# Kernel optimization log

Measured on AMD Instinct MI355X. Metric: run time of the kernel, lower is better.

Reference implementation:

```python
import jax, jax.numpy as jnp
import numpy as np

B, S, H = 2, 1024, 2048
E, K, F = 64, 8, 768
CAP = 512


def setup_inputs() -> dict:
    key = jax.random.key(0)
    k1, k2, k3, k4, k5 = jax.random.split(key, 5)
    scale_h = 1.0 / np.sqrt(H)
    scale_f = 1.0 / np.sqrt(F)
    return {
        "hidden_states": jax.random.normal(k1, (B, S, H), jnp.float32),
        "router_w": jax.random.normal(k2, (E, H), jnp.float32) * scale_h,   # MoEGate.weight [E, H]
        "w_gate": jax.random.normal(k3, (E, H, F), jnp.float32) * scale_h,
        "w_up": jax.random.normal(k4, (E, H, F), jnp.float32) * scale_h,
        "w_down": jax.random.normal(k5, (E, F, H), jnp.float32) * scale_f,
    }


def reference(hidden_states, router_w, w_gate, w_up, w_down):
    b, s, h = hidden_states.shape
    T = b * s
    xf = hidden_states.reshape(T, h)

    # --- MoEGate: softmax over expert logits, then top-k, then renormalize ---
    logits = xf @ router_w.T                                   # [T, E]
    scores = jax.nn.softmax(logits.astype(jnp.float32), axis=-1)
    topk_w, topk_idx = jax.lax.top_k(scores, K)                # [T, K]
    topk_w = topk_w / (topk_w.sum(axis=-1, keepdims=True) + 1e-20)

    # --- dispatch: scatter each (token, k) slot into a per-expert capacity buffer ---
    slot_expert = topk_idx.reshape(-1)                         # [T*K]
    slot_token = jnp.repeat(jnp.arange(T), K)                  # [T*K]
    onehot = jax.nn.one_hot(slot_expert, E, dtype=jnp.int32)   # [T*K, E]
    pos = (jnp.cumsum(onehot, axis=0) * onehot).sum(-1) - 1    # position within expert
    valid = pos < CAP
    dest = jnp.where(valid, slot_expert * CAP + pos, E * CAP)  # overflow -> dummy row

    buf = jnp.zeros((E * CAP + 1, h), xf.dtype).at[dest].set(xf[slot_token])
    xb = buf[: E * CAP].reshape(E, CAP, h)                     # [E, CAP, H]

    # --- grouped GEMM experts: SwiGLU MLP per expert ---
    gate = jnp.einsum("ech,ehf->ecf", xb, w_gate)
    up = jnp.einsum("ech,ehf->ecf", xb, w_up)
    hmid = jax.nn.silu(gate) * up                              # [E, CAP, F]
    yb = jnp.einsum("ecf,efh->ech", hmid, w_down).reshape(E * CAP, h)
    yb = jnp.concatenate([yb, jnp.zeros((1, h), yb.dtype)], axis=0)

    # --- combine: gather expert outputs back, weight, scatter-add per token ---
    slot_out = yb[dest] * topk_w.reshape(-1)[:, None].astype(yb.dtype)
    out = jnp.zeros((T, h), yb.dtype).at[slot_token].add(slot_out)
    return out.reshape(b, s, h)
```

## Files before the change

kernel.cpp:

```cpp
#include <hip/hip_runtime.h>
#include <math.h>

#define T_TOK 2048
#define HD    2048
#define NEXP  64
#define KTOP  8
#define FD    768
#define CAPE  512

typedef float  f32x4 __attribute__((ext_vector_type(4)));
typedef __bf16 bf16x8 __attribute__((ext_vector_type(8)));
typedef __bf16 bf16x4 __attribute__((ext_vector_type(4)));

__device__ __forceinline__ void load_lds16(const void* g, void* l) {
  __builtin_amdgcn_global_load_lds(
      (const __attribute__((address_space(1))) unsigned int*)g,
      (__attribute__((address_space(3))) unsigned int*)l, 16, 0, 0);
}

#define WAITCNT(S) asm volatile(S ::: "memory")
#define PIN()      asm volatile("" ::: "memory")
#define BARRIER()  __builtin_amdgcn_s_barrier()

__global__ __launch_bounds__(256) void router_kernel(
    const float* __restrict__ x, const float* __restrict__ rw,
    int* __restrict__ cnt, int* __restrict__ tok_list, float* __restrict__ w_list,
    unsigned short* __restrict__ xb)
{
  const int t = threadIdx.x;
  const int tb = blockIdx.x * 4;
  __shared__ float xs[4][HD];
  __shared__ float lg[4][NEXP];

  const float4* xsrc = (const float4*)(x + (size_t)tb * HD);
  float4* xdst = (float4*)&xs[0][0];
  for (int i = t; i < 4 * HD / 4; i += 256) xdst[i] = xsrc[i];
  __syncthreads();

  {
    const int e = t >> 2, q = t & 3;
    const float* wrow = rw + (size_t)e * HD;
    float a0 = 0.f, a1 = 0.f, a2 = 0.f, a3 = 0.f;
    for (int i = 0; i < HD / 16; ++i) {
      int h = (i * 4 + q) * 4;
      float4 wv = *(const float4*)(wrow + h);
      float4 x0 = *(const float4*)&xs[0][h];
      float4 x1 = *(const float4*)&xs[1][h];
      float4 x2 = *(const float4*)&xs[2][h];
      float4 x3 = *(const float4*)&xs[3][h];
      a0 += wv.x*x0.x + wv.y*x0.y + wv.z*x0.z + wv.w*x0.w;
      a1 += wv.x*x1.x + wv.y*x1.y + wv.z*x1.z + wv.w*x1.w;
      a2 += wv.x*x2.x + wv.y*x2.y + wv.z*x2.z + wv.w*x2.w;
      a3 += wv.x*x3.x + wv.y*x3.y + wv.z*x3.z + wv.w*x3.w;
    }
    a0 += __shfl_xor(a0, 1); a0 += __shfl_xor(a0, 2);
    a1 += __shfl_xor(a1, 1); a1 += __shfl_xor(a1, 2);
    a2 += __shfl_xor(a2, 1); a2 += __shfl_xor(a2, 2);
    a3 += __shfl_xor(a3, 1); a3 += __shfl_xor(a3, 2);
    if (q == 0) { lg[0][e] = a0; lg[1][e] = a1; lg[2][e] = a2; lg[3][e] = a3; }
  }

  {
    const f32x4* xs4 = (const f32x4*)(x + (size_t)tb * HD);
    bf16x4* xbd = (bf16x4*)(xb + (size_t)tb * HD);
    #pragma unroll
    for (int j = 0; j < 8; ++j) {
      f32x4 v = xs4[j * 256 + t];
      xbd[j * 256 + t] = (bf16x4){(__bf16)v[0], (__bf16)v[1], (__bf16)v[2], (__bf16)v[3]};
    }
  }
  __syncthreads();

  const int wid = t >> 6, lane = t & 63;
  float v = lg[wid][lane];
  float mx = v;
  for (int o = 32; o; o >>= 1) mx = fmaxf(mx, __shfl_xor(mx, o));
  float p = expf(v - mx);
  float s = p;
  for (int o = 32; o; o >>= 1) s += __shfl_xor(s, o);
  float prob = p / s;

  float r = prob;
  float wk[KTOP]; int ik[KTOP]; float wsum = 0.f;
  #pragma unroll
  for (int k = 0; k < KTOP; ++k) {
    float bv = r; int bl = lane;
    for (int o = 32; o; o >>= 1) {
      float ov = __shfl_xor(bv, o); int ol = __shfl_xor(bl, o);
      if (ov > bv || (ov == bv && ol < bl)) { bv = ov; bl = ol; }
    }
    wk[k] = bv; ik[k] = bl; wsum += bv;
    if (lane == bl) r = -1.f;
  }
  if (lane == 0) {
    float inv = 1.f / (wsum + 1e-20f);
    int token = tb + wid;
    #pragma unroll
    for (int k = 0; k < KTOP; ++k) {
      int ex = ik[k];
      int pos = atomicAdd(&cnt[ex], 1);
      if (pos < CAPE) {
        tok_list[ex * CAPE + pos] = token;
        w_list[ex * CAPE + pos] = wk[k] * inv;
      }
    }
  }
}


__global__ __launch_bounds__(512, 4) void gateup_kernel(
    const unsigned short* __restrict__ xb,
    const float* __restrict__ wg, const float* __restrict__ wu,
    const int* __restrict__ cnt, const int* __restrict__ tok_list,
    unsigned short* __restrict__ hmid)
{
  const int nt = blockIdx.x, mt = blockIdx.y, e = blockIdx.z;
  int ne = cnt[e]; ne = ne < CAPE ? ne : CAPE;
  if (mt * 128 >= ne) return;
  const int t = threadIdx.x, lane = t & 63, wid = t >> 6;
  const int wr = wid >> 1, wc = wid & 1;

  __shared__ __align__(16) unsigned short A[2 * 128 * 64];
  __shared__ __align__(16) unsigned short Bg[64 * 72];
  __shared__ __align__(16) unsigned short Bu[64 * 72];
  __shared__ int toks[128];

  if (t < 128) {
    int r = mt * 128 + t;
    toks[t] = tok_list[e * CAPE + (r < ne ? r : 0)];
  }
  __syncthreads();

  const unsigned short* asrc[2];
  #pragma unroll
  for (int i = 0; i < 2; ++i) {
    const int inst = wid * 2 + i;
    const int G = inst * 64 + lane;
    const int m = G >> 3, gg = G & 7;
    asrc[i] = xb + (size_t)toks[m] * HD + 8 * (gg ^ (m & 7));
  }

  f32x4 z4 = {0.f, 0.f, 0.f, 0.f};
  f32x4 gacc[2][2], uacc[2][2];
  #pragma unroll
  for (int i = 0; i < 2; ++i)
    #pragma unroll
    for (int j = 0; j < 2; ++j) { gacc[i][j] = z4; uacc[i][j] = z4; }

  const int bq = t & 255, nc = bq & 15, kc = bq >> 4;
  const float* wsel = (wid < 4) ? wg : wu;
  __bf16* bsel = (wid < 4) ? (__bf16*)Bg : (__bf16*)Bu;
  const size_t wbase = (size_t)e * HD * FD + (size_t)nt * 64;
  f32x4 Ra[4], Rb[4];

#define LOAD_GU(K0, R) do { \
    const float* p_ = wsel + wbase + (size_t)((K0) + kc * 4) * FD + nc * 4; \
    R[0] = *(const f32x4*)p_;            R[1] = *(const f32x4*)(p_ + FD); \
    R[2] = *(const f32x4*)(p_ + 2*FD);   R[3] = *(const f32x4*)(p_ + 3*FD); \
  } while (0)

#define STAGE_A2(KT, BUF) do { \
    const int k0s_ = (KT) * 64; \
    load_lds16(asrc[0] + k0s_, &A[(BUF) * 8192 + (wid * 2 + 0) * 512]); \
    load_lds16(asrc[1] + k0s_, &A[(BUF) * 8192 + (wid * 2 + 1) * 512]); \
  } while (0)

#define CVT_GU(R) do { \
    const int xm_ = (nc & 7) << 3; \
    _Pragma("unroll") \
    for (int j_ = 0; j_ < 4; ++j_) { \
      int so_ = (nc * 4 + j_) * 72 + ((kc * 4) ^ xm_); \
      *(bf16x4*)&bsel[so_] = (bf16x4){(__bf16)R[0][j_], (__bf16)R[1][j_], (__bf16)R[2][j_], (__bf16)R[3][j_]}; \
    } \
  } while (0)

#define COMPUTE_GU(CUR) do { \
    const char* Ab_ = (const char*)&A[(CUR) * 8192]; \
    const __bf16* Bg_ = (const __bf16*)Bg; \
    const __bf16* Bu_ = (const __bf16*)Bu; \
    _Pragma("unroll") \
    for (int ks = 0; ks < 2; ++ks) { \
      bf16x8 af[2]; \
      _Pragma("unroll") \
      for (int mf = 0; mf < 2; ++mf) { \
        int row = wr * 32 + mf * 16 + (lane & 15); \
        int byte = row * 128 + (lane >> 4) * 16 + ks * 64; \
        byte ^= (row & 7) << 4; \
        af[mf] = *(const bf16x8*)(Ab_ + byte); \
      } \
      _Pragma("unroll") \
      for (int nf = 0; nf < 2; ++nf) { \
        int n = wc * 32 + nf * 16 + (lane & 15); \
        int so = n * 72 + ((((lane >> 4) * 8) + ks * 32) ^ (((n >> 2) & 7) << 3)); \
        bf16x8 bgf = *(const bf16x8*)&Bg_[so]; \
        bf16x8 bum = *(const bf16x8*)&Bu_[so]; \
        _Pragma("unroll") \
        for (int mf = 0; mf < 2; ++mf) { \
          gacc[mf][nf] = __builtin_amdgcn_mfma_f32_16x16x32_bf16(af[mf], bgf, gacc[mf][nf], 0, 0, 0); \
          uacc[mf][nf] = __builtin_amdgcn_mfma_f32_16x16x32_bf16(af[mf], bum, uacc[mf][nf], 0, 0, 0); \
        } \
      } \
    } \
  } while (0)

  LOAD_GU(0, Ra);
  PIN();
  STAGE_A2(0, 0);
  PIN();
  LOAD_GU(64, Rb);
  WAITCNT("s_waitcnt vmcnt(6)");
  CVT_GU(Ra);
  WAITCNT("s_waitcnt vmcnt(4) lgkmcnt(0)");
  BARRIER();

  for (int i = 0; i < 15; ++i) {
    const int kt = 2 * i;
    STAGE_A2(kt + 1, 1);
    PIN();
    LOAD_GU((kt + 2) * 64, Ra);
    COMPUTE_GU(0);
    WAITCNT("s_waitcnt lgkmcnt(0)");
    BARRIER();
    WAITCNT("s_waitcnt vmcnt(6)");
    CVT_GU(Rb);
    WAITCNT("s_waitcnt vmcnt(4) lgkmcnt(0)");
    BARRIER();
    STAGE_A2(kt + 2, 0);
    PIN();
    LOAD_GU((kt + 3) * 64, Rb);
    COMPUTE_GU(1);
    WAITCNT("s_waitcnt lgkmcnt(0)");
    BARRIER();
    WAITCNT("s_waitcnt vmcnt(6)");
    CVT_GU(Ra);
    WAITCNT("s_waitcnt vmcnt(4) lgkmcnt(0)");
    BARRIER();
  }
  STAGE_A2(31, 1);
  COMPUTE_GU(0);
  WAITCNT("s_waitcnt lgkmcnt(0)");
  BARRIER();
  WAITCNT("s_waitcnt vmcnt(2)");
  CVT_GU(Rb);
  WAITCNT("s_waitcnt vmcnt(0) lgkmcnt(0)");
  BARRIER();
  COMPUTE_GU(1);

#undef LOAD_GU
#undef STAGE_A2
#undef CVT_GU
#undef COMPUTE_GU

  const size_t hbase = (size_t)e * CAPE + (size_t)mt * 128;
  __bf16* hm = (__bf16*)hmid;
  #pragma unroll
  for (int mf = 0; mf < 2; ++mf) {
    #pragma unroll
    for (int nf = 0; nf < 2; ++nf) {
      #pragma unroll
      for (int r = 0; r < 4; ++r) {
        int row = wr * 32 + mf * 16 + (lane >> 4) * 4 + r;
        int c = nt * 64 + wc * 32 + nf * 16 + (lane & 15);
        float gv = gacc[mf][nf][r], uv = uacc[mf][nf][r];
        float hv = gv / (1.f + __expf(-gv)) * uv;
        hm[(hbase + row) * FD + c] = (__bf16)hv;
      }
    }
  }
}

__global__ __launch_bounds__(512, 4) void down_kernel(
    const unsigned short* __restrict__ hmid,
    const float* __restrict__ wd,
    const int* __restrict__ cnt, const int* __restrict__ tok_list,
    const float* __restrict__ w_list, float* __restrict__ out)
{
  const int nt = blockIdx.x, mt = blockIdx.y, e = blockIdx.z;
  int ne = cnt[e]; ne = ne < CAPE ? ne : CAPE;
  if (mt * 128 >= ne) return;
  const int t = threadIdx.x, lane = t & 63, wid = t >> 6;
  const int wr = wid >> 1, wc = wid & 1;

  __shared__ __align__(16) unsigned short A[2 * 128 * 64];
  __shared__ __align__(16) unsigned short Bd[64 * 72];
  __shared__ int toks[128];
  __shared__ float wts[128];

  if (t < 128) {
    int r = mt * 128 + t;
    bool vv = r < ne;
    toks[t] = vv ? tok_list[e * CAPE + r] : 0;
    wts[t]  = vv ? w_list[e * CAPE + r] : 0.f;
  }
  __syncthreads();

  const size_t arow = (size_t)e * CAPE + (size_t)mt * 128;
  const unsigned short* asrc[2];
  #pragma unroll
  for (int i = 0; i < 2; ++i) {
    const int inst = wid * 2 + i;
    const int G = inst * 64 + lane;
    const int m = G >> 3, gg = G & 7;
    asrc[i] = hmid + (arow + m) * FD + 8 * (gg ^ (m & 7));
  }

  f32x4 z4 = {0.f, 0.f, 0.f, 0.f};
  f32x4 dacc[2][2];
  #pragma unroll
  for (int i = 0; i < 2; ++i)
    #pragma unroll
    for (int j = 0; j < 2; ++j) dacc[i][j] = z4;

  const int bq = t & 255, nc = bq & 15, kc = bq >> 4;
  const size_t wbase = (size_t)e * FD * HD + (size_t)nt * 64;
  f32x4 Ra[4], Rb[4];

#define LOAD_D(K0, R) do { \
    const float* p_ = wd + wbase + (size_t)((K0) + kc * 4) * HD + nc * 4; \
    R[0] = *(const f32x4*)p_;            R[1] = *(const f32x4*)(p_ + HD); \
    R[2] = *(const f32x4*)(p_ + 2*HD);   R[3] = *(const f32x4*)(p_ + 3*HD); \
  } while (0)

#define STAGE_A2(KT, BUF) do { \
    const int k0s_ = (KT) * 64; \
    load_lds16(asrc[0] + k0s_, &A[(BUF) * 8192 + (wid * 2 + 0) * 512]); \
    load_lds16(asrc[1] + k0s_, &A[(BUF) * 8192 + (wid * 2 + 1) * 512]); \
  } while (0)

#define CVT_D(R) do { \
    __bf16* bd_ = (__bf16*)Bd; \
    const int xm_ = (nc & 7) << 3; \
    _Pragma("unroll") \
    for (int j_ = 0; j_ < 4; ++j_) { \
      int so_ = (nc * 4 + j_) * 72 + ((kc * 4) ^ xm_); \
      *(bf16x4*)&bd_[so_] = (bf16x4){(__bf16)R[0][j_], (__bf16)R[1][j_], (__bf16)R[2][j_], (__bf16)R[3][j_]}; \
    } \
  } while (0)

#define COMPUTE_D(CUR) do { \
    const char* Ab_ = (const char*)&A[(CUR) * 8192]; \
    const __bf16* Bd_ = (const __bf16*)Bd; \
    _Pragma("unroll") \
    for (int ks = 0; ks < 2; ++ks) { \
      bf16x8 af[2]; \
      _Pragma("unroll") \
      for (int mf = 0; mf < 2; ++mf) { \
        int row = wr * 32 + mf * 16 + (lane & 15); \
        int byte = row * 128 + (lane >> 4) * 16 + ks * 64; \
        byte ^= (row & 7) << 4; \
        af[mf] = *(const bf16x8*)(Ab_ + byte); \
      } \
      _Pragma("unroll") \
      for (int nf = 0; nf < 2; ++nf) { \
        int n = wc * 32 + nf * 16 + (lane & 15); \
        int so = n * 72 + ((((lane >> 4) * 8) + ks * 32) ^ (((n >> 2) & 7) << 3)); \
        bf16x8 bdf = *(const bf16x8*)&Bd_[so]; \
        _Pragma("unroll") \
        for (int mf = 0; mf < 2; ++mf) \
          dacc[mf][nf] = __builtin_amdgcn_mfma_f32_16x16x32_bf16(af[mf], bdf, dacc[mf][nf], 0, 0, 0); \
      } \
    } \
  } while (0)

  if (wid < 4) LOAD_D(0, Ra);
  PIN();
  STAGE_A2(0, 0);
  PIN();
  if (wid < 4) {
    LOAD_D(64, Rb);
    WAITCNT("s_waitcnt vmcnt(6)");
    CVT_D(Ra);
    WAITCNT("s_waitcnt vmcnt(4) lgkmcnt(0)");
  } else {
    WAITCNT("s_waitcnt vmcnt(0) lgkmcnt(0)");
  }
  BARRIER();

  for (int i = 0; i < 5; ++i) {
    const int kt = 2 * i;
    STAGE_A2(kt + 1, 1);
    PIN();
    if (wid < 4) LOAD_D((kt + 2) * 64, Ra);
    COMPUTE_D(0);
    WAITCNT("s_waitcnt lgkmcnt(0)");
    BARRIER();
    if (wid < 4) {
      WAITCNT("s_waitcnt vmcnt(6)");
      CVT_D(Rb);
      WAITCNT("s_waitcnt vmcnt(4) lgkmcnt(0)");
    } else {
      WAITCNT("s_waitcnt vmcnt(0) lgkmcnt(0)");
    }
    BARRIER();

    STAGE_A2(kt + 2, 0);
    PIN();
    if (wid < 4) LOAD_D((kt + 3) * 64, Rb);
    COMPUTE_D(1);
    WAITCNT("s_waitcnt lgkmcnt(0)");
    BARRIER();
    if (wid < 4) {
      WAITCNT("s_waitcnt vmcnt(6)");
      CVT_D(Ra);
      WAITCNT("s_waitcnt vmcnt(4) lgkmcnt(0)");
    } else {
      WAITCNT("s_waitcnt vmcnt(0) lgkmcnt(0)");
    }
    BARRIER();
  }
  STAGE_A2(11, 1);
  COMPUTE_D(0);
  WAITCNT("s_waitcnt lgkmcnt(0)");
  BARRIER();
  if (wid < 4) {
    WAITCNT("s_waitcnt vmcnt(2)");
    CVT_D(Rb);
    WAITCNT("s_waitcnt vmcnt(0) lgkmcnt(0)");
  } else {
    WAITCNT("s_waitcnt vmcnt(0) lgkmcnt(0)");
  }
  BARRIER();
  COMPUTE_D(1);

#undef LOAD_D
#undef STAGE_A2
#undef CVT_D
#undef COMPUTE_D

  #pragma unroll
  for (int mf = 0; mf < 2; ++mf) {
    #pragma unroll
    for (int nf = 0; nf < 2; ++nf) {
      int c = nt * 64 + wc * 32 + nf * 16 + (lane & 15);
      #pragma unroll
      for (int r = 0; r < 4; ++r) {
        int row = wr * 32 + mf * 16 + (lane >> 4) * 4 + r;
        if (mt * 128 + row < ne) {
          int tok = toks[row];
          float w = wts[row];
          atomicAdd(&out[(size_t)tok * HD + c], w * dacc[mf][nf][r]);
        }
      }
    }
  }
}

extern "C" void kernel_launch(void* const* d_in, const int* in_sizes, int n_in,
                              void* d_out, int out_size, void* d_ws, size_t ws_size,
                              hipStream_t stream) {
  const float* x  = (const float*)d_in[0];
  const float* rw = (const float*)d_in[1];
  const float* wg = (const float*)d_in[2];
  const float* wu = (const float*)d_in[3];
  const float* wd = (const float*)d_in[4];
  float* out = (float*)d_out;

  char* ws = (char*)d_ws;
  unsigned short* xb   = (unsigned short*)ws;
  int* cnt             = (int*)(ws + 8388608);
  int* tok_list        = (int*)(ws + 8388864);
  float* w_list        = (float*)(ws + 8519936);
  unsigned short* hmid = (unsigned short*)(ws + 8651008);

  hipMemsetAsync(d_out, 0, (size_t)out_size * sizeof(float), stream);
  hipMemsetAsync(cnt, 0, NEXP * sizeof(int), stream);

  router_kernel<<<T_TOK / 4, 256, 0, stream>>>(x, rw, cnt, tok_list, w_list, xb);
  gateup_kernel<<<dim3(FD / 64, CAPE / 128, NEXP), 512, 0, stream>>>(xb, wg, wu, cnt, tok_list, hmid);
  down_kernel<<<dim3(HD / 64, CAPE / 128, NEXP), 512, 0, stream>>>(hmid, wd, cnt, tok_list, w_list, out);
}
```

Baseline: 706.9 us.

## Double-buffer weight LDS tiles, remap block order for XCD locality, spread down loads

Gives the B (weight) tiles in both MoE GEMM kernels two LDS buffers, so the bf16 conversion of the next tile overlaps the MFMA compute on the current one. This removes one barrier per k-step. Block IDs are flattened into a 1D grid and remapped so consecutive blocks on the same XCD (bid&7) cover neighbouring m-tiles of the same expert and n-tile, which should improve L2 reuse of weights. The down kernel now spreads its weight loads across all 8 waves instead of 4 and raises its occupancy hint to 6, at the cost of more LDS per block.

```diff
diff --git a/kernel.cpp b/kernel.cpp
--- a/kernel.cpp
+++ b/kernel.cpp
@@ -11,6 +11,7 @@
 typedef float  f32x4 __attribute__((ext_vector_type(4)));
 typedef __bf16 bf16x8 __attribute__((ext_vector_type(8)));
 typedef __bf16 bf16x4 __attribute__((ext_vector_type(4)));
+typedef __bf16 bf16x2 __attribute__((ext_vector_type(2)));
 
 __device__ __forceinline__ void load_lds16(const void* g, void* l) {
   __builtin_amdgcn_global_load_lds(
@@ -114,15 +115,18 @@
     const int* __restrict__ cnt, const int* __restrict__ tok_list,
     unsigned short* __restrict__ hmid)
 {
-  const int nt = blockIdx.x, mt = blockIdx.y, e = blockIdx.z;
+  const int bid = blockIdx.x;
+  const int d = (bid & 7) * 384 + (bid >> 3);
+  const int mt = d & 3, nt = (d >> 2) % 12, e = d / 48;
+
   int ne = cnt[e]; ne = ne < CAPE ? ne : CAPE;
   if (mt * 128 >= ne) return;
   const int t = threadIdx.x, lane = t & 63, wid = t >> 6;
   const int wr = wid >> 1, wc = wid & 1;
 
   __shared__ __align__(16) unsigned short A[2 * 128 * 64];
-  __shared__ __align__(16) unsigned short Bg[64 * 72];
-  __shared__ __align__(16) unsigned short Bu[64 * 72];
+  __shared__ __align__(16) unsigned short Bg[2 * 64 * 72];
+  __shared__ __align__(16) unsigned short Bu[2 * 64 * 72];
   __shared__ int toks[128];
 
   if (t < 128) {
@@ -165,19 +169,20 @@
     load_lds16(asrc[1] + k0s_, &A[(BUF) * 8192 + (wid * 2 + 1) * 512]); \
   } while (0)
 
-#define CVT_GU(R) do { \
+#define CVT_GU(BUF, R) do { \
+    __bf16* b_ = bsel + (BUF) * 4608; \
     const int xm_ = (nc & 7) << 3; \
     _Pragma("unroll") \
     for (int j_ = 0; j_ < 4; ++j_) { \
       int so_ = (nc * 4 + j_) * 72 + ((kc * 4) ^ xm_); \
-      *(bf16x4*)&bsel[so_] = (bf16x4){(__bf16)R[0][j_], (__bf16)R[1][j_], (__bf16)R[2][j_], (__bf16)R[3][j_]}; \
+      *(bf16x4*)&b_[so_] = (bf16x4){(__bf16)R[0][j_], (__bf16)R[1][j_], (__bf16)R[2][j_], (__bf16)R[3][j_]}; \
     } \
   } while (0)
 
 #define COMPUTE_GU(CUR) do { \
     const char* Ab_ = (const char*)&A[(CUR) * 8192]; \
-    const __bf16* Bg_ = (const __bf16*)Bg; \
-    const __bf16* Bu_ = (const __bf16*)Bu; \
+    const __bf16* Bg_ = (const __bf16*)&Bg[(CUR) * 4608]; \
+    const __bf16* Bu_ = (const __bf16*)&Bu[(CUR) * 4608]; \
     _Pragma("unroll") \
     for (int ks = 0; ks < 2; ++ks) { \
       bf16x8 af[2]; \
@@ -209,7 +214,7 @@
   PIN();
   LOAD_GU(64, Rb);
   WAITCNT("s_waitcnt vmcnt(6)");
-  CVT_GU(Ra);
+  CVT_GU(0, Ra);
   WAITCNT("s_waitcnt vmcnt(4) lgkmcnt(0)");
   BARRIER();
 
@@ -218,30 +223,24 @@
     STAGE_A2(kt + 1, 1);
     PIN();
     LOAD_GU((kt + 2) * 64, Ra);
+    WAITCNT("s_waitcnt vmcnt(6)");
+    CVT_GU(1, Rb);
     COMPUTE_GU(0);
-    WAITCNT("s_waitcnt lgkmcnt(0)");
-    BARRIER();
-    WAITCNT("s_waitcnt vmcnt(6)");
-    CVT_GU(Rb);
     WAITCNT("s_waitcnt vmcnt(4) lgkmcnt(0)");
     BARRIER();
     STAGE_A2(kt + 2, 0);
     PIN();
     LOAD_GU((kt + 3) * 64, Rb);
+    WAITCNT("s_waitcnt vmcnt(6)");
+    CVT_GU(0, Ra);
     COMPUTE_GU(1);
-    WAITCNT("s_waitcnt lgkmcnt(0)");
-    BARRIER();
-    WAITCNT("s_waitcnt vmcnt(6)");
-    CVT_GU(Ra);
     WAITCNT("s_waitcnt vmcnt(4) lgkmcnt(0)");
     BARRIER();
   }
   STAGE_A2(31, 1);
+  WAITCNT("s_waitcnt vmcnt(2)");
+  CVT_GU(1, Rb);
   COMPUTE_GU(0);
-  WAITCNT("s_waitcnt lgkmcnt(0)");
-  BARRIER();
-  WAITCNT("s_waitcnt vmcnt(2)");
-  CVT_GU(Rb);
   WAITCNT("s_waitcnt vmcnt(0) lgkmcnt(0)");
   BARRIER();
   COMPUTE_GU(1);
@@ -269,20 +268,23 @@
   }
 }
 
-__global__ __launch_bounds__(512, 4) void down_kernel(
+__global__ __launch_bounds__(512, 6) void down_kernel(
     const unsigned short* __restrict__ hmid,
     const float* __restrict__ wd,
     const int* __restrict__ cnt, const int* __restrict__ tok_list,
     const float* __restrict__ w_list, float* __restrict__ out)
 {
-  const int nt = blockIdx.x, mt = blockIdx.y, e = blockIdx.z;
+  const int bid = blockIdx.x;
+  const int d = (bid & 7) * 1024 + (bid >> 3);
+  const int mt = d & 3, nt = (d >> 2) & 31, e = d >> 7;
+
   int ne = cnt[e]; ne = ne < CAPE ? ne : CAPE;
   if (mt * 128 >= ne) return;
   const int t = threadIdx.x, lane = t & 63, wid = t >> 6;
   const int wr = wid >> 1, wc = wid & 1;
 
   __shared__ __align__(16) unsigned short A[2 * 128 * 64];
-  __shared__ __align__(16) unsigned short Bd[64 * 72];
+  __shared__ __align__(16) unsigned short Bd[2 * 64 * 72];
   __shared__ int toks[128];
   __shared__ float wts[128];
 
@@ -311,14 +313,13 @@
     #pragma unroll
     for (int j = 0; j < 2; ++j) dacc[i][j] = z4;
 
-  const int bq = t & 255, nc = bq & 15, kc = bq >> 4;
+  const int nc = t & 15, kc2 = t >> 4;
   const size_t wbase = (size_t)e * FD * HD + (size_t)nt * 64;
-  f32x4 Ra[4], Rb[4];
+  f32x4 Ra[2], Rb[2];
 
 #define LOAD_D(K0, R) do { \
-    const float* p_ = wd + wbase + (size_t)((K0) + kc * 4) * HD + nc * 4; \
-    R[0] = *(const f32x4*)p_;            R[1] = *(const f32x4*)(p_ + HD); \
-    R[2] = *(const f32x4*)(p_ + 2*HD);   R[3] = *(const f32x4*)(p_ + 3*HD); \
+    const float* p_ = wd + wbase + (size_t)((K0) + kc2 * 2) * HD + nc * 4; \
+    R[0] = *(const f32x4*)p_;  R[1] = *(const f32x4*)(p_ + HD); \
   } while (0)
 
 #define STAGE_A2(KT, BUF) do { \
@@ -327,19 +328,19 @@
     load_lds16(asrc[1] + k0s_, &A[(BUF) * 8192 + (wid * 2 + 1) * 512]); \
   } while (0)
 
-#define CVT_D(R) do { \
-    __bf16* bd_ = (__bf16*)Bd; \
+#define CVT_D(BUF, R) do { \
+    __bf16* bd_ = (__bf16*)&Bd[(BUF) * 4608]; \
     const int xm_ = (nc & 7) << 3; \
     _Pragma("unroll") \
     for (int j_ = 0; j_ < 4; ++j_) { \
-      int so_ = (nc * 4 + j_) * 72 + ((kc * 4) ^ xm_); \
-      *(bf16x4*)&bd_[so_] = (bf16x4){(__bf16)R[0][j_], (__bf16)R[1][j_], (__bf16)R[2][j_], (__bf16)R[3][j_]}; \
+      int so_ = (nc * 4 + j_) * 72 + ((kc2 * 2) ^ xm_); \
+      *(bf16x2*)&bd_[so_] = (bf16x2){(__bf16)R[0][j_], (__bf16)R[1][j_]}; \
     } \
   } while (0)
 
 #define COMPUTE_D(CUR) do { \
     const char* Ab_ = (const char*)&A[(CUR) * 8192]; \
-    const __bf16* Bd_ = (const __bf16*)Bd; \
+    const __bf16* Bd_ = (const __bf16*)&Bd[(CUR) * 4608]; \
     _Pragma("unroll") \
     for (int ks = 0; ks < 2; ++ks) { \
       bf16x8 af[2]; \
@@ -362,63 +363,41 @@
     } \
   } while (0)
 
-  if (wid < 4) LOAD_D(0, Ra);
+  LOAD_D(0, Ra);
   PIN();
   STAGE_A2(0, 0);
   PIN();
-  if (wid < 4) {
-    LOAD_D(64, Rb);
-    WAITCNT("s_waitcnt vmcnt(6)");
-    CVT_D(Ra);
-    WAITCNT("s_waitcnt vmcnt(4) lgkmcnt(0)");
-  } else {
-    WAITCNT("s_waitcnt vmcnt(0) lgkmcnt(0)");
-  }
+  LOAD_D(64, Rb);
+  WAITCNT("s_waitcnt vmcnt(4)");
+  CVT_D(0, Ra);
+  WAITCNT("s_waitcnt vmcnt(2) lgkmcnt(0)");
   BARRIER();
 
   for (int i = 0; i < 5; ++i) {
     const int kt = 2 * i;
     STAGE_A2(kt + 1, 1);
     PIN();
-    if (wid < 4) LOAD_D((kt + 2) * 64, Ra);
+    LOAD_D((kt + 2) * 64, Ra);
+    WAITCNT("s_waitcnt vmcnt(4)");
+    CVT_D(1, Rb);
     COMPUTE_D(0);
-    WAITCNT("s_waitcnt lgkmcnt(0)");
-    BARRIER();
-    if (wid < 4) {
-      WAITCNT("s_waitcnt vmcnt(6)");
-      CVT_D(Rb);
-      WAITCNT("s_waitcnt vmcnt(4) lgkmcnt(0)");
-    } else {
-      WAITCNT("s_waitcnt vmcnt(0) lgkmcnt(0)");
-    }
+    WAITCNT("s_waitcnt vmcnt(2) lgkmcnt(0)");
     BARRIER();
 
     STAGE_A2(kt + 2, 0);
     PIN();
-    if (wid < 4) LOAD_D((kt + 3) * 64, Rb);
+    LOAD_D((kt + 3) * 64, Rb);
+    WAITCNT("s_waitcnt vmcnt(4)");
+    CVT_D(0, Ra);
     COMPUTE_D(1);
-    WAITCNT("s_waitcnt lgkmcnt(0)");
+    WAITCNT("s_waitcnt vmcnt(2) lgkmcnt(0)");
     BARRIER();
-    if (wid < 4) {
-      WAITCNT("s_waitcnt vmcnt(6)");
-      CVT_D(Ra);
-      WAITCNT("s_waitcnt vmcnt(4) lgkmcnt(0)");
-    } else {
-      WAITCNT("s_waitcnt vmcnt(0) lgkmcnt(0)");
-    }
-    BARRIER();
   }
   STAGE_A2(11, 1);
+  WAITCNT("s_waitcnt vmcnt(2)");
+  CVT_D(1, Rb);
   COMPUTE_D(0);
-  WAITCNT("s_waitcnt lgkmcnt(0)");
-  BARRIER();
-  if (wid < 4) {
-    WAITCNT("s_waitcnt vmcnt(2)");
-    CVT_D(Rb);
-    WAITCNT("s_waitcnt vmcnt(0) lgkmcnt(0)");
-  } else {
-    WAITCNT("s_waitcnt vmcnt(0) lgkmcnt(0)");
-  }
+  WAITCNT("s_waitcnt vmcnt(0) lgkmcnt(0)");
   BARRIER();
   COMPUTE_D(1);
 
@@ -466,6 +445,6 @@
   hipMemsetAsync(cnt, 0, NEXP * sizeof(int), stream);
 
   router_kernel<<<T_TOK / 4, 256, 0, stream>>>(x, rw, cnt, tok_list, w_list, xb);
-  gateup_kernel<<<dim3(FD / 64, CAPE / 128, NEXP), 512, 0, stream>>>(xb, wg, wu, cnt, tok_list, hmid);
-  down_kernel<<<dim3(HD / 64, CAPE / 128, NEXP), 512, 0, stream>>>(hmid, wd, cnt, tok_list, w_list, out);
+  gateup_kernel<<<3072, 512, 0, stream>>>(xb, wg, wu, cnt, tok_list, hmid);
+  down_kernel<<<8192, 512, 0, stream>>>(hmid, wd, cnt, tok_list, w_list, out);
 }
```

Result: slower. 750.6 us (+6.2%).
